# Optimization experiments

Measured on AMD Instinct MI355X. Metric: run time of the kernel, lower is better.

Reference implementation:

```python
import jax, jax.numpy as jnp
import numpy as np

N, E, IN, OUT, T = 50000, 800000, 16, 16, 8
LN_EPS = 1e-5


def setup_inputs() -> dict:
    key = jax.random.key(0)
    ks = jax.random.split(key, 8)
    x = jax.random.normal(ks[0], (N, IN), dtype=jnp.float32)
    edge_index = jax.random.randint(ks[1], (2, E), 0, N, dtype=jnp.int64)
    edge_attr = jax.random.normal(ks[2], (E, T), dtype=jnp.float32)
    # LayerNorm params
    ln_gamma = jnp.ones((IN,), dtype=jnp.float32)
    ln_beta = jnp.zeros((IN,), dtype=jnp.float32)
    # edge_nn: Linear(t, in*out)
    w_edge = jax.random.normal(ks[3], (T, IN * OUT), dtype=jnp.float32) * (1.0 / np.sqrt(T))
    b_edge = jax.random.normal(ks[4], (IN * OUT,), dtype=jnp.float32) * 0.01
    # NNConv root weight [in, out] and bias [out]
    root = jax.random.normal(ks[5], (IN, OUT), dtype=jnp.float32) * (1.0 / np.sqrt(IN))
    bias = jax.random.normal(ks[6], (OUT,), dtype=jnp.float32) * 0.01
    return {"x": x, "edge_index": edge_index, "edge_attr": edge_attr,
            "ln_gamma": ln_gamma, "ln_beta": ln_beta,
            "w_edge": w_edge, "b_edge": b_edge, "root": root, "bias": bias}


def reference(x, edge_index, edge_attr, ln_gamma, ln_beta, w_edge, b_edge, root, bias):
    # pre: LayerNorm -> ReLU (Dropout is identity in eval mode)
    mu = jnp.mean(x, axis=-1, keepdims=True)
    var = jnp.mean((x - mu) ** 2, axis=-1, keepdims=True)
    h = (x - mu) * jax.lax.rsqrt(var + LN_EPS) * ln_gamma + ln_beta
    h = jax.nn.relu(h)  # [N, IN]

    # edge MLP -> per-edge weight matrices [E, IN, OUT]
    theta = (edge_attr @ w_edge + b_edge).reshape(E, IN, OUT)

    src = edge_index[0]  # message source j
    dst = edge_index[1]  # aggregation target i (PyG source_to_target flow)

    # per-edge matmul: x_j [E, IN] x theta [E, IN, OUT] -> [E, OUT]
    msg = jnp.einsum('ei,eio->eo', h[src], theta)

    # scatter-add into target nodes
    agg = jax.ops.segment_sum(msg, dst, num_segments=N)  # [N, OUT]

    # root transform + bias
    out = agg + h @ root + bias
    return out
```

## Files before the change

kernel.cpp:

```cpp
#include <hip/hip_runtime.h>
#include <hip/hip_fp16.h>

#define N_NODES 50000
#define E_EDGES 800000
#define NTILES  (E_EDGES / 16)

typedef __attribute__((ext_vector_type(8))) short short8;
typedef __attribute__((ext_vector_type(4))) float floatx4;

__device__ __forceinline__ short f2bf(float x) {
    union { float f; unsigned u; } v; v.f = x;
    unsigned r = v.u + 0x7FFFu + ((v.u >> 16) & 1u);
    return (short)(r >> 16);
}

__device__ __forceinline__ unsigned pk_bf16(float lo, float hi) {
    union { float f; unsigned u; } a, b; a.f = lo; b.f = hi;
    return __builtin_amdgcn_perm(b.u, a.u, 0x07060302u);
}

__global__ __launch_bounds__(256) void node_kernel(
    const float* __restrict__ x, const float* __restrict__ gamma,
    const float* __restrict__ beta, const float* __restrict__ root,
    const float* __restrict__ bias, float* __restrict__ h,
    float* __restrict__ out, __half* __restrict__ agg)
{
    int n = blockIdx.x * blockDim.x + threadIdx.x;
    if (n >= N_NODES) return;
    const float* xr = x + n * 16;
    float xv[16];
    #pragma unroll
    for (int i = 0; i < 4; ++i) ((floatx4*)xv)[i] = ((const floatx4*)xr)[i];
    float mu = 0.f;
    #pragma unroll
    for (int i = 0; i < 16; ++i) mu += xv[i];
    mu *= (1.f / 16.f);
    float var = 0.f;
    #pragma unroll
    for (int i = 0; i < 16; ++i) { float d = xv[i] - mu; var += d * d; }
    var *= (1.f / 16.f);
    float rs = rsqrtf(var + 1e-5f);
    float hv[16];
    #pragma unroll
    for (int i = 0; i < 16; ++i) {
        float t = (xv[i] - mu) * rs * gamma[i] + beta[i];
        hv[i] = t > 0.f ? t : 0.f;
    }
    float* hr = h + n * 16;
    #pragma unroll
    for (int i = 0; i < 4; ++i) ((floatx4*)hr)[i] = ((floatx4*)hv)[i];

    floatx4 z = {0.f, 0.f, 0.f, 0.f};
    floatx4* az = (floatx4*)(agg + (size_t)n * 16);
    az[0] = z; az[1] = z;

    float ov[16];
    #pragma unroll
    for (int o = 0; o < 16; ++o) ov[o] = bias[o];
    #pragma unroll
    for (int i = 0; i < 16; ++i) {
        float hi = hv[i];
        #pragma unroll
        for (int o = 0; o < 16; ++o) ov[o] += hi * root[i * 16 + o];
    }
    float* orow = out + n * 16;
    #pragma unroll
    for (int i = 0; i < 4; ++i) ((floatx4*)orow)[i] = ((floatx4*)ov)[i];
}

__global__ __launch_bounds__(256) void prep_kernel(
    const float* __restrict__ w_edge, const float* __restrict__ b_edge,
    short* __restrict__ w2t)
{
    int t = blockIdx.x * blockDim.x + threadIdx.x;
    if (t >= 16 * 160) return;
    int m = t / 160, k = t % 160;
    float v = 0.f;
    if (k < 128)      v = w_edge[(k >> 4) * 256 + (k & 15) * 16 + m];
    else if (k < 144) v = b_edge[(k - 128) * 16 + m];
    w2t[m * 160 + k] = f2bf(v);
}

__global__ __launch_bounds__(256) void edge_kernel(
    const int* __restrict__ eidx, const float* __restrict__ ea,
    const short* __restrict__ w2t, const float* __restrict__ h,
    __half* __restrict__ agg)
{
    const int lane = threadIdx.x & 63;
    const int wid  = threadIdx.x >> 6;
    const int m = lane & 15;
    const int q = lane >> 4;

    const int tile = blockIdx.x * 4 + wid;
    if (tile >= NTILES) return;

    const int e   = tile * 16 + m;
    const int src = eidx[e];
    const int dst = eidx[E_EDGES + e];

    const short* wp = w2t + m * 160 + 8 * q;
    short8 bfrag[5];
    #pragma unroll
    for (int c = 0; c < 5; ++c)
        bfrag[c] = *(const short8*)(wp + 32 * c);

    const float* er = ea + (size_t)e * 8;
    floatx4 ea0 = ((const floatx4*)er)[0];
    floatx4 ea1 = ((const floatx4*)er)[1];

    const float* hr = h + src * 16 + 8 * (q & 1);
    floatx4 h0 = ((const floatx4*)hr)[0];
    floatx4 h1 = ((const floatx4*)hr)[1];
    float hh[8] = {h0.x, h0.y, h0.z, h0.w, h1.x, h1.y, h1.z, h1.w};

    floatx4 acc = {0.f, 0.f, 0.f, 0.f};
    const int hi_t = q >> 1;
    #pragma unroll
    for (int c = 0; c < 4; ++c) {
        float t_even, t_odd;
        if (c == 0)      { t_even = ea0.x; t_odd = ea0.y; }
        else if (c == 1) { t_even = ea0.z; t_odd = ea0.w; }
        else if (c == 2) { t_even = ea1.x; t_odd = ea1.y; }
        else             { t_even = ea1.z; t_odd = ea1.w; }
        float s = hi_t ? t_odd : t_even;
        union { short8 s8; unsigned u[4]; } af;
        #pragma unroll
        for (int p = 0; p < 4; ++p)
            af.u[p] = pk_bf16(s * hh[2 * p], s * hh[2 * p + 1]);
        acc = __builtin_amdgcn_mfma_f32_16x16x32_bf16(af.s8, bfrag[c], acc, 0, 0, 0);
    }
    {
        const unsigned msk = (q < 2) ? 0xFFFFFFFFu : 0u;
        union { short8 s8; unsigned u[4]; } af;
        #pragma unroll
        for (int p = 0; p < 4; ++p)
            af.u[p] = pk_bf16(hh[2 * p], hh[2 * p + 1]) & msk;
        acc = __builtin_amdgcn_mfma_f32_16x16x32_bf16(af.s8, bfrag[4], acc, 0, 0, 0);
    }

    const int odd = m & 1;
    const int mlo = m & ~1;
    #pragma unroll
    for (int r = 0; r < 4; ++r) {
        float p  = __shfl_xor(acc[r], 1, 64);
        float lo = odd ? p : acc[r];
        float hi = odd ? acc[r] : p;
        __half2 v = __floats2half2_rn(lo, hi);
        int dr = __shfl(dst, 4 * q + r, 64);
        if ((r >> 1) == odd)
            unsafeAtomicAdd((__half2*)(agg + (size_t)dr * 16 + mlo), v);
    }
}

__global__ __launch_bounds__(256) void merge_kernel(
    const __half* __restrict__ agg, float* __restrict__ out)
{
    int n = blockIdx.x * blockDim.x + threadIdx.x;
    if (n >= N_NODES) return;
    const __half2* ar = (const __half2*)(agg + (size_t)n * 16);
    float* orow = out + (size_t)n * 16;
    floatx4 o[4];
    #pragma unroll
    for (int i = 0; i < 4; ++i) o[i] = ((floatx4*)orow)[i];
    #pragma unroll
    for (int j = 0; j < 8; ++j) {
        float2 f = __half22float2(ar[j]);
        o[j / 2][(j & 1) * 2 + 0] += f.x;
        o[j / 2][(j & 1) * 2 + 1] += f.y;
    }
    #pragma unroll
    for (int i = 0; i < 4; ++i) ((floatx4*)orow)[i] = o[i];
}

extern "C" void kernel_launch(void* const* d_in, const int* in_sizes, int n_in,
                              void* d_out, int out_size, void* d_ws, size_t ws_size,
                              hipStream_t stream) {
    const float* x        = (const float*)d_in[0];
    const int*   eidx     = (const int*)d_in[1];
    const float* ea       = (const float*)d_in[2];
    const float* ln_gamma = (const float*)d_in[3];
    const float* ln_beta  = (const float*)d_in[4];
    const float* w_edge   = (const float*)d_in[5];
    const float* b_edge   = (const float*)d_in[6];
    const float* root     = (const float*)d_in[7];
    const float* bias     = (const float*)d_in[8];
    float* out = (float*)d_out;

    char* ws = (char*)d_ws;
    float*  h   = (float*)ws;
    short*  w2t = (short*)(ws + (size_t)N_NODES * 16 * 4);
    __half* agg = (__half*)(ws + (size_t)N_NODES * 16 * 4 + 16 * 160 * 2);

    prep_kernel<<<10, 256, 0, stream>>>(w_edge, b_edge, w2t);
    node_kernel<<<(N_NODES + 255) / 256, 256, 0, stream>>>(
        x, ln_gamma, ln_beta, root, bias, h, out, agg);
    edge_kernel<<<(NTILES + 3) / 4, 256, 0, stream>>>(eidx, ea, w2t, h, agg);
    merge_kernel<<<(N_NODES + 255) / 256, 256, 0, stream>>>(agg, out);
}
```

Baseline: 136.0 us.

## Process four edge tiles per wave with batched loads and direct dst fetch

```diff
diff --git a/kernel.cpp b/kernel.cpp
--- a/kernel.cpp
+++ b/kernel.cpp
@@ -4,6 +4,7 @@
 #define N_NODES 50000
 #define E_EDGES 800000
 #define NTILES  (E_EDGES / 16)
+#define TPW 4
 
 typedef __attribute__((ext_vector_type(8))) short short8;
 typedef __attribute__((ext_vector_type(4))) float floatx4;
@@ -81,7 +82,7 @@
     w2t[m * 160 + k] = f2bf(v);
 }
 
-__global__ __launch_bounds__(256) void edge_kernel(
+__global__ __launch_bounds__(256, 4) void edge_kernel(
     const int* __restrict__ eidx, const float* __restrict__ ea,
     const short* __restrict__ w2t, const float* __restrict__ h,
     __half* __restrict__ agg)
@@ -90,13 +91,11 @@
     const int wid  = threadIdx.x >> 6;
     const int m = lane & 15;
     const int q = lane >> 4;
-
-    const int tile = blockIdx.x * 4 + wid;
-    if (tile >= NTILES) return;
-
-    const int e   = tile * 16 + m;
-    const int src = eidx[e];
-    const int dst = eidx[E_EDGES + e];
+    const int odd = m & 1;
+    const int mlo = m & ~1;
+
+    const int tile0 = (blockIdx.x * 4 + wid) * TPW;
+    if (tile0 >= NTILES) return;
 
     const short* wp = w2t + m * 160 + 8 * q;
     short8 bfrag[5];
@@ -104,51 +103,69 @@
     for (int c = 0; c < 5; ++c)
         bfrag[c] = *(const short8*)(wp + 32 * c);
 
-    const float* er = ea + (size_t)e * 8;
-    floatx4 ea0 = ((const floatx4*)er)[0];
-    floatx4 ea1 = ((const floatx4*)er)[1];
-
-    const float* hr = h + src * 16 + 8 * (q & 1);
-    floatx4 h0 = ((const floatx4*)hr)[0];
-    floatx4 h1 = ((const floatx4*)hr)[1];
-    float hh[8] = {h0.x, h0.y, h0.z, h0.w, h1.x, h1.y, h1.z, h1.w};
-
-    floatx4 acc = {0.f, 0.f, 0.f, 0.f};
+    int src[TPW];
+    int2 d2[TPW];
+    floatx4 e0[TPW], e1[TPW];
+    #pragma unroll
+    for (int t = 0; t < TPW; ++t) {
+        const int e = (tile0 + t) * 16 + m;
+        src[t] = eidx[e];
+        d2[t] = *(const int2*)(eidx + E_EDGES + (tile0 + t) * 16 + 4 * q + 2 * odd);
+        const float* er = ea + (size_t)e * 8;
+        e0[t] = ((const floatx4*)er)[0];
+        e1[t] = ((const floatx4*)er)[1];
+    }
+
+    floatx4 g0[TPW], g1[TPW];
+    #pragma unroll
+    for (int t = 0; t < TPW; ++t) {
+        const float* hr = h + src[t] * 16 + 8 * (q & 1);
+        g0[t] = ((const floatx4*)hr)[0];
+        g1[t] = ((const floatx4*)hr)[1];
+    }
+
     const int hi_t = q >> 1;
     #pragma unroll
-    for (int c = 0; c < 4; ++c) {
-        float t_even, t_odd;
-        if (c == 0)      { t_even = ea0.x; t_odd = ea0.y; }
-        else if (c == 1) { t_even = ea0.z; t_odd = ea0.w; }
-        else if (c == 2) { t_even = ea1.x; t_odd = ea1.y; }
-        else             { t_even = ea1.z; t_odd = ea1.w; }
-        float s = hi_t ? t_odd : t_even;
-        union { short8 s8; unsigned u[4]; } af;
-        #pragma unroll
-        for (int p = 0; p < 4; ++p)
-            af.u[p] = pk_bf16(s * hh[2 * p], s * hh[2 * p + 1]);
-        acc = __builtin_amdgcn_mfma_f32_16x16x32_bf16(af.s8, bfrag[c], acc, 0, 0, 0);
-    }
-    {
-        const unsigned msk = (q < 2) ? 0xFFFFFFFFu : 0u;
-        union { short8 s8; unsigned u[4]; } af;
-        #pragma unroll
-        for (int p = 0; p < 4; ++p)
-            af.u[p] = pk_bf16(hh[2 * p], hh[2 * p + 1]) & msk;
-        acc = __builtin_amdgcn_mfma_f32_16x16x32_bf16(af.s8, bfrag[4], acc, 0, 0, 0);
-    }
-
-    const int odd = m & 1;
-    const int mlo = m & ~1;
-    #pragma unroll
-    for (int r = 0; r < 4; ++r) {
-        float p  = __shfl_xor(acc[r], 1, 64);
-        float lo = odd ? p : acc[r];
-        float hi = odd ? acc[r] : p;
-        __half2 v = __floats2half2_rn(lo, hi);
-        int dr = __shfl(dst, 4 * q + r, 64);
-        if ((r >> 1) == odd)
+    for (int t = 0; t < TPW; ++t) {
+        float hh[8] = {g0[t].x, g0[t].y, g0[t].z, g0[t].w,
+                       g1[t].x, g1[t].y, g1[t].z, g1[t].w};
+        floatx4 acc = {0.f, 0.f, 0.f, 0.f};
+        #pragma unroll
+        for (int c = 0; c < 4; ++c) {
+            float te, to;
+            if (c == 0)      { te = e0[t].x; to = e0[t].y; }
+            else if (c == 1) { te = e0[t].z; to = e0[t].w; }
+            else if (c == 2) { te = e1[t].x; to = e1[t].y; }
+            else             { te = e1[t].z; to = e1[t].w; }
+            float s = hi_t ? to : te;
+            union { short8 s8; unsigned u[4]; } af;
+            #pragma unroll
+            for (int p = 0; p < 4; ++p)
+                af.u[p] = pk_bf16(s * hh[2 * p], s * hh[2 * p + 1]);
+            acc = __builtin_amdgcn_mfma_f32_16x16x32_bf16(af.s8, bfrag[c], acc, 0, 0, 0);
+        }
+        {
+            const unsigned msk = (q < 2) ? 0xFFFFFFFFu : 0u;
+            union { short8 s8; unsigned u[4]; } af;
+            #pragma unroll
+            for (int p = 0; p < 4; ++p)
+                af.u[p] = pk_bf16(hh[2 * p], hh[2 * p + 1]) & msk;
+            acc = __builtin_amdgcn_mfma_f32_16x16x32_bf16(af.s8, bfrag[4], acc, 0, 0, 0);
+        }
+
+        float px[4];
+        #pragma unroll
+        for (int r = 0; r < 4; ++r)
+            px[r] = __shfl_xor(acc[r], 1, 64);
+        #pragma unroll
+        for (int k = 0; k < 2; ++k) {
+            const int r = 2 * odd + k;
+            float lo = odd ? px[r] : acc[r];
+            float hi = odd ? acc[r] : px[r];
+            __half2 v = __floats2half2_rn(lo, hi);
+            const int dr = k ? d2[t].y : d2[t].x;
             unsafeAtomicAdd((__half2*)(agg + (size_t)dr * 16 + mlo), v);
+        }
     }
 }
 
@@ -194,6 +211,7 @@
     prep_kernel<<<10, 256, 0, stream>>>(w_edge, b_edge, w2t);
     node_kernel<<<(N_NODES + 255) / 256, 256, 0, stream>>>(
         x, ln_gamma, ln_beta, root, bias, h, out, agg);
-    edge_kernel<<<(NTILES + 3) / 4, 256, 0, stream>>>(eidx, ea, w2t, h, agg);
+    edge_kernel<<<(NTILES + 4 * TPW - 1) / (4 * TPW), 256, 0, stream>>>(
+        eidx, ea, w2t, h, agg);
     merge_kernel<<<(N_NODES + 255) / 256, 256, 0, stream>>>(agg, out);
 }
```

Result: slower. 145.8 us (+7.2%).
